# Kernel tuning notes

Measured on AMD Instinct MI355X. Metric: run time of the kernel, lower is better.

## Reference

```python
import jax, jax.numpy as jnp
import numpy as np

V, D, M = 13000, 300, 500   # vocab, embed dim, cell/mem size (hardcoded in source)
B, NW, T = 64, 5, 128       # episodes, ways, seq len
EPS = 1e-8                  # torch cosine_similarity default eps


def setup_inputs():
    key = jax.random.key(0)
    ks = jax.random.split(key, 14)
    s = 0.05  # xavier-ish scale
    return {
        "support_tokens": jax.random.randint(ks[0], (B, NW, T), 0, V, dtype=jnp.int32),
        "target_tokens": jax.random.randint(ks[1], (B, T), 0, V, dtype=jnp.int32),
        "blank_pos_support": jax.random.randint(ks[2], (B, NW), 0, T, dtype=jnp.int32),
        "blank_pos_target": jax.random.randint(ks[3], (B,), 0, T, dtype=jnp.int32),
        "target_y": jax.random.randint(ks[4], (B,), 0, NW, dtype=jnp.int32),
        "emb": jax.random.normal(ks[5], (V, D)) * s,
        "WL": jax.random.normal(ks[6], (3, M, D)) * s,
        "UL": jax.random.normal(ks[7], (3, M, M)) * s,
        "bL": jnp.zeros((3, M)),
        "WR": jax.random.normal(ks[8], (3, M, D)) * s,
        "UR": jax.random.normal(ks[9], (3, M, M)) * s,
        "bR": jnp.zeros((3, M)),
        "Wo": jax.random.normal(ks[10], (D, M)) * s,
        "Uo": jax.random.normal(ks[11], (D, M)) * s,
        "bo": jnp.zeros((D,)),
        "c0L": jnp.zeros((M,)),
        "c0R": jnp.zeros((M,)),
    }


def _cell_scan(x, W, U, b, c0):
    # x: [T, D] -> pre-update cell states (the 'env' the source appends BEFORE updating _c): [T, M]
    gx = jnp.einsum('td,gmd->tgm', x, W) + b  # input projections for all 3 gates, all timesteps
    def step(c, g):
        g = g + jnp.einsum('gmh,h->gm', U, c)
        f = jax.nn.sigmoid(g[0])
        i = jax.nn.sigmoid(g[1])
        cbar = jnp.tanh(g[2])
        return f * c + i * cbar, c
    _, pre = jax.lax.scan(step, c0, gx)
    return pre


def _blank_env(tokens, blank_pos, emb, WL, UL, bL, WR, UR, bR, Wo, Uo, bo, c0L, c0R):
    # tokens: [N, T], blank_pos: [N] -> env vector at blank position: [N, D]
    x = emb[tokens]  # [N, T, D]
    Lenv = jax.vmap(lambda xs: _cell_scan(xs, WL, UL, bL, c0L))(x)          # [N, T, M]
    Renv = jax.vmap(lambda xs: _cell_scan(xs[::-1], WR, UR, bR, c0R))(x)[:, ::-1]
    n = jnp.arange(tokens.shape[0])
    l = Lenv[n, blank_pos]  # [N, M]
    r = Renv[n, blank_pos]  # source pairs Lenv[i] with Renv[T-1-i] of the reversed list == right pre-state at pos i
    return jnp.tanh(l @ Wo.T + r @ Uo.T + bo)  # oNN: unbatched_Linear(lev=0, tanh)


def reference(support_tokens, target_tokens, blank_pos_support, blank_pos_target,
              target_y, emb, WL, UL, bL, WR, UR, bR, Wo, Uo, bo, c0L, c0R):
    b, nw, t = support_tokens.shape
    sup = _blank_env(support_tokens.reshape(b * nw, t), blank_pos_support.reshape(b * nw),
                     emb, WL, UL, bL, WR, UR, bR, Wo, Uo, bo, c0L, c0R).reshape(b, nw, -1)
    tgt = _blank_env(target_tokens, blank_pos_target,
                     emb, WL, UL, bL, WR, UR, bR, Wo, Uo, bo, c0L, c0R)  # [B, D]
    # cosine similarity per way, scaled by 10 (fce LSTM output is discarded in the source, so omitted)
    dot = jnp.einsum('bnd,bd->bn', sup, tgt)
    denom = jnp.maximum(jnp.linalg.norm(sup, axis=-1) * jnp.linalg.norm(tgt, axis=-1)[:, None], EPS)
    z = (dot / denom) * 10.0  # [B, NW]
    probs = jax.nn.softmax(z, axis=1)
    accuracy = jnp.mean((jnp.argmax(probs, axis=1) == target_y).astype(jnp.float32))
    # F.cross_entropy applied to the softmax probs (double softmax), as in the source
    logp = jax.nn.log_softmax(probs, axis=1)
    loss = -jnp.mean(jnp.take_along_axis(logp, target_y[:, None].astype(jnp.int32), axis=1))
    return accuracy, loss
```

## Files before the change

### kernel.cpp

```cpp
#include <hip/hip_runtime.h>
#include <math.h>

#define V 13000
#define D 300
#define M 500
#define B 64
#define NW 5
#define T 128
#define NSUP (B*NW)
#define NSEQ (NSUP + B)
#define CT 32
#define NCT 12
#define MT 16
#define NMT 32
#define KSPL 4
#define CHK 20
#define CKS 10
#define XCH 15
#define NSTEP (T-1)
#define ASZ (KSPL*CHK*MT*4)
#define BSZ (KSPL*CHK*CT)

__device__ __forceinline__ float sigmoidf_(float x){ return 1.0f/(1.0f+expf(-x)); }


__global__ void init_kernel(const float* __restrict__ c0L, const float* __restrict__ c0R,
                            float* __restrict__ actB0, float* __restrict__ c_final)
{
    int idx = blockIdx.x*256 + threadIdx.x;
    if (idx >= 2*M*NSEQ) return;
    int d = idx / (M*NSEQ);
    int rem = idx % (M*NSEQ);
    int m = rem / NSEQ;
    int r = rem % NSEQ;
    float v = d ? c0R[m] : c0L[m];
    actB0[((size_t)d*M + m)*NSEQ + r] = v;
    c_final[((size_t)d*NSEQ + r)*M + m] = v;
}

__global__ void sort_kernel(const int* __restrict__ blank_sup, const int* __restrict__ blank_tgt,
                            int* __restrict__ perm, int* __restrict__ lenR, int* __restrict__ tmax)
{
    __shared__ int L0[NSEQ], L1[NSEQ];
    int tid = threadIdx.x;
    int blank = (tid < NSUP) ? blank_sup[tid] : blank_tgt[tid - NSUP];
    int l0 = blank, l1 = (T-1) - blank;
    L0[tid] = l0; L1[tid] = l1;
    __syncthreads();
    int r0 = 0, r1 = 0;
    for (int j = 0; j < NSEQ; ++j) {
        int c = L0[j]; r0 += (c > l0) || (c == l0 && j < tid);
        int d = L1[j]; r1 += (d > l1) || (d == l1 && j < tid);
    }
    perm[r0] = tid;        lenR[r0] = l0;
    perm[NSEQ + r1] = tid; lenR[NSEQ + r1] = l1;
    __syncthreads();
    if (tid < 2*NCT) {
        int dir = tid / NCT, t = tid % NCT;
        tmax[tid] = lenR[dir*NSEQ + t*CT];
    }
}

__global__ __launch_bounds__(256)
void step_kernel(int s,
                 const float* __restrict__ actB_cur, float* __restrict__ actB_next,
                 float* __restrict__ c_final,
                 const float* __restrict__ WL, const float* __restrict__ UL, const float* __restrict__ bL,
                 const float* __restrict__ WR, const float* __restrict__ UR, const float* __restrict__ bR,
                 const int* __restrict__ perm, const int* __restrict__ lenR, const int* __restrict__ tmax,
                 const int* __restrict__ sup_tok, const int* __restrict__ tgt_tok,
                 const float* __restrict__ emb)
{
    const int bid = blockIdx.x;
    const int ct = bid >> 6;
    const int dm = bid & 63;
    const int d  = dm >> 5;
    const int mt = dm & 31;
    if (s >= tmax[d*NCT + ct]) return;

    __shared__ float smem[ASZ + BSZ];
    __shared__ int tok_s[CT], len_s[CT];

    const int tid  = threadIdx.x;
    const int ks   = tid >> 6;
    const int lane = tid & 63;
    const int ty   = lane >> 3;
    const int tx   = lane & 7;
    const int rank0 = ct*CT;

    if (tid < CT) {
        int rank = rank0 + tid;
        int ch = perm[d*NSEQ + rank];
        len_s[tid] = lenR[d*NSEQ + rank];
        int tpos = d ? (T-1-s) : s;
        tok_s[tid] = (ch < NSUP) ? sup_tok[ch*T + tpos] : tgt_tok[(ch-NSUP)*T + tpos];
    }
    __syncthreads();

    const float* Wd = d ? WR : WL;
    const float* Ud = d ? UR : UL;
    const float* bias = d ? bR : bL;

    float* As = smem;
    float* Bs = smem + ASZ;

    float acc[2][3][4];
    #pragma unroll
    for (int j=0;j<2;++j)
        #pragma unroll
        for (int g=0;g<3;++g)
            #pragma unroll
            for (int c=0;c<4;++c) acc[j][g][c] = 0.f;

    float4 aR[4];
    float4 bR4[3];

    auto loadA = [&](int gc){
        const bool isx = (gc < XCH);
        const int k0 = gc*CHK;
        #pragma unroll
        for (int i=0;i<4;++i){
            int slot = lane + 64*i;
            if (slot < 240){
                int row = slot/5, kq = slot%5;
                int g = row >> 4, ml = row & 15;
                int m = mt*MT + ml;
                float4 v = make_float4(0.f,0.f,0.f,0.f);
                if (m < M){
                    const float* src = isx ? (Wd + (size_t)(g*M + m)*D + k0 + kq*4)
                                           : (Ud + (size_t)(g*M + m)*M + (k0-300) + kq*4);
                    v = *(const float4*)src;
                }
                aR[i] = v;
            }
        }
    };
    auto loadB = [&](int gc){
        const int k0 = gc*CHK;
        if (gc < XCH){
            #pragma unroll
            for (int i=0;i<3;++i){
                int slot = lane + 64*i;
                if (slot < 160){
                    int c = slot/5, kq = slot%5;
                    bR4[i] = *(const float4*)(emb + (size_t)tok_s[c]*D + k0 + kq*4);
                }
            }
        } else {
            #pragma unroll
            for (int i=0;i<3;++i){
                int slot = lane + 64*i;
                if (slot < 160){
                    int kk = slot >> 3, c4 = slot & 7;
                    bR4[i] = *(const float4*)(actB_cur + ((size_t)d*M + (k0-300) + kk)*NSEQ + rank0 + c4*4);
                }
            }
        }
    };
    auto writeAB = [&](int gc){
        #pragma unroll
        for (int i=0;i<4;++i){
            int slot = lane + 64*i;
            if (slot < 240){
                int row = slot/5, kq = slot%5;
                int g = row >> 4, ml = row & 15;
                float4 v = aR[i];
                As[((ks*CHK + kq*4+0)*MT + ml)*4 + g] = v.x;
                As[((ks*CHK + kq*4+1)*MT + ml)*4 + g] = v.y;
                As[((ks*CHK + kq*4+2)*MT + ml)*4 + g] = v.z;
                As[((ks*CHK + kq*4+3)*MT + ml)*4 + g] = v.w;
            }
        }
        if (gc < XCH){
            #pragma unroll
            for (int i=0;i<3;++i){
                int slot = lane + 64*i;
                if (slot < 160){
                    int c = slot/5, kq = slot%5;
                    float4 v = bR4[i];
                    Bs[(ks*CHK + kq*4+0)*CT + c] = v.x;
                    Bs[(ks*CHK + kq*4+1)*CT + c] = v.y;
                    Bs[(ks*CHK + kq*4+2)*CT + c] = v.z;
                    Bs[(ks*CHK + kq*4+3)*CT + c] = v.w;
                }
            }
        } else {
            #pragma unroll
            for (int i=0;i<3;++i){
                int slot = lane + 64*i;
                if (slot < 160){
                    int kk = slot >> 3, c4 = slot & 7;
                    *(float4*)&Bs[(ks*CHK + kk)*CT + c4*4] = bR4[i];
                }
            }
        }
    };

#define FMA4(AC, AV, BV) AC[0] += (AV)*(BV).x; AC[1] += (AV)*(BV).y; AC[2] += (AV)*(BV).z; AC[3] += (AV)*(BV).w;

    loadA(ks*CKS); loadB(ks*CKS);
    for (int ck = 0; ck < CKS; ++ck){
        const int gc = ks*CKS + ck;
        writeAB(gc);
        if (ck + 1 < CKS){ loadA(gc+1); loadB(gc+1); }
        #pragma unroll
        for (int kk = 0; kk < CHK; ++kk){
            float4 a0 = *(const float4*)&As[((ks*CHK + kk)*MT + ty*2    )*4];
            float4 a1 = *(const float4*)&As[((ks*CHK + kk)*MT + ty*2 + 1)*4];
            float4 b  = *(const float4*)&Bs[(ks*CHK + kk)*CT + tx*4];
            FMA4(acc[0][0], a0.x, b);
            FMA4(acc[0][1], a0.y, b);
            FMA4(acc[0][2], a0.z, b);
            FMA4(acc[1][0], a1.x, b);
            FMA4(acc[1][1], a1.y, b);
            FMA4(acc[1][2], a1.z, b);
        }
    }

    __syncthreads();
    float* red = smem;
    #pragma unroll
    for (int j=0;j<2;++j){
        int ml = ty*2 + j;
        #pragma unroll
        for (int g=0;g<3;++g){
            *(float4*)&red[((ks*MT + ml)*3 + g)*CT + tx*4] =
                make_float4(acc[j][g][0], acc[j][g][1], acc[j][g][2], acc[j][g][3]);
        }
    }
    __syncthreads();

    #pragma unroll
    for (int q=0;q<2;++q){
        int cell = tid*2 + q;
        int ml = cell >> 5, c = cell & 31;
        int m = mt*MT + ml;
        if (m < M){
            float g0 = bias[m], g1 = bias[M + m], g2 = bias[2*M + m];
            #pragma unroll
            for (int kq=0;kq<KSPL;++kq){
                g0 += red[((kq*MT + ml)*3 + 0)*CT + c];
                g1 += red[((kq*MT + ml)*3 + 1)*CT + c];
                g2 += red[((kq*MT + ml)*3 + 2)*CT + c];
            }
            int rank = rank0 + c;
            int len  = len_s[c];
            size_t cidx = ((size_t)d*M + m)*NSEQ + rank;
            float cold = actB_cur[cidx];
            float f  = sigmoidf_(g0);
            float i2 = sigmoidf_(g1);
            float cb = tanhf(g2);
            float cn = (s < len) ? (f*cold + i2*cb) : cold;
            actB_next[cidx] = cn;
            if (s == len - 1){
                int ch = perm[d*NSEQ + rank];
                c_final[((size_t)d*NSEQ + ch)*M + m] = cn;
            }
        }
    }
#undef FMA4
}

__global__ void env_kernel(const float* __restrict__ l_states, const float* __restrict__ r_states,
                           const float* __restrict__ Wo, const float* __restrict__ Uo,
                           const float* __restrict__ bo,
                           float* __restrict__ env)
{
    __shared__ __align__(16) float l[M];
    __shared__ __align__(16) float r[M];
    const int i = blockIdx.x;
    const int tid = threadIdx.x;
    for (int m=tid; m<M; m+=blockDim.x){ l[m]=l_states[i*M+m]; r[m]=r_states[i*M+m]; }
    __syncthreads();
    for (int d=tid; d<D; d+=blockDim.x) {
        const float4* wo = reinterpret_cast<const float4*>(Wo + (size_t)d*M);
        const float4* uo = reinterpret_cast<const float4*>(Uo + (size_t)d*M);
        const float4* lv = reinterpret_cast<const float4*>(l);
        const float4* rv = reinterpret_cast<const float4*>(r);
        float acc = bo[d];
        #pragma unroll 5
        for (int q=0; q<M/4; ++q) {
            float4 a=wo[q], bv=lv[q], u=uo[q], rr=rv[q];
            acc += a.x*bv.x + a.y*bv.y + a.z*bv.z + a.w*bv.w;
            acc += u.x*rr.x + u.y*rr.y + u.z*rr.z + u.w*rr.w;
        }
        env[i*D + d] = tanhf(acc);
    }
}

__global__ void episode_kernel(const float* __restrict__ env, const int* __restrict__ target_y,
                               float* __restrict__ flags, float* __restrict__ losses)
{
    const int b = blockIdx.x;
    const int lane = threadIdx.x;
    const float* tgt = env + (size_t)(NSUP + b)*D;

    float tn = 0.f;
    for (int d=lane; d<D; d+=64){ float v=tgt[d]; tn += v*v; }
    for (int off=32; off; off>>=1) tn += __shfl_down(tn, off);
    tn = __shfl(tn, 0);

    float z[NW];
    for (int n=0; n<NW; ++n){
        const float* sup = env + (size_t)(b*NW + n)*D;
        float dot=0.f, sn=0.f;
        for (int d=lane; d<D; d+=64){ float sv=sup[d], tv=tgt[d]; dot+=sv*tv; sn+=sv*sv; }
        for (int off=32; off; off>>=1){ dot += __shfl_down(dot,off); sn += __shfl_down(sn,off); }
        dot = __shfl(dot,0); sn = __shfl(sn,0);
        float denom = fmaxf(sqrtf(sn)*sqrtf(tn), 1e-8f);
        z[n] = dot/denom*10.0f;
    }

    if (lane==0){
        float mx=z[0];
        for(int n=1;n<NW;n++) mx=fmaxf(mx,z[n]);
        float se=0.f; float p[NW];
        for(int n=0;n<NW;n++){ p[n]=expf(z[n]-mx); se+=p[n]; }
        for(int n=0;n<NW;n++) p[n]/=se;
        int am=0; float bv=p[0];
        for(int n=1;n<NW;n++) if(p[n]>bv){bv=p[n];am=n;}
        int y = target_y[b];
        flags[b] = (am==y)?1.0f:0.0f;
        float mx2=p[0]; for(int n=1;n<NW;n++) mx2=fmaxf(mx2,p[n]);
        float se2=0.f; for(int n=0;n<NW;n++) se2+=expf(p[n]-mx2);
        losses[b] = -(p[y]-mx2-logf(se2));
    }
}

__global__ void finalize_kernel(const float* __restrict__ flags, const float* __restrict__ losses,
                                float* __restrict__ out)
{
    const int lane = threadIdx.x;
    float f = flags[lane], l = losses[lane];
    for (int off=32; off; off>>=1){ f += __shfl_down(f,off); l += __shfl_down(l,off); }
    if (lane==0){ out[0] = f/(float)B; out[1] = l/(float)B; }
}

extern "C" void kernel_launch(void* const* d_in, const int* in_sizes, int n_in,
                              void* d_out, int out_size, void* d_ws, size_t ws_size,
                              hipStream_t stream) {
    const int*   sup_tok   = (const int*)d_in[0];
    const int*   tgt_tok   = (const int*)d_in[1];
    const int*   blank_sup = (const int*)d_in[2];
    const int*   blank_tgt = (const int*)d_in[3];
    const int*   target_y  = (const int*)d_in[4];
    const float* emb = (const float*)d_in[5];
    const float* WL  = (const float*)d_in[6];
    const float* UL  = (const float*)d_in[7];
    const float* bL  = (const float*)d_in[8];
    const float* WR  = (const float*)d_in[9];
    const float* UR  = (const float*)d_in[10];
    const float* bR  = (const float*)d_in[11];
    const float* Wo  = (const float*)d_in[12];
    const float* Uo  = (const float*)d_in[13];
    const float* bo  = (const float*)d_in[14];
    const float* c0L = (const float*)d_in[15];
    const float* c0R = (const float*)d_in[16];

    float* ws_f = (float*)d_ws;
    float* actB0   = ws_f;
    float* actB1   = actB0 + 2*M*NSEQ;
    float* c_final = actB1 + 2*M*NSEQ;
    float* env     = c_final + 2*NSEQ*M;
    float* flags   = env + NSEQ*D;
    float* losses  = flags + B;
    int*   perm    = (int*)(losses + B);
    int*   lenR    = perm + 2*NSEQ;
    int*   tmax    = lenR + 2*NSEQ;

    init_kernel<<<(2*M*NSEQ + 255)/256, 256, 0, stream>>>(c0L, c0R, actB0, c_final);
    sort_kernel<<<1, NSEQ, 0, stream>>>(blank_sup, blank_tgt, perm, lenR, tmax);

    for (int s = 0; s < NSTEP; ++s) {
        float* cur  = (s & 1) ? actB1 : actB0;
        float* next = (s & 1) ? actB0 : actB1;
        step_kernel<<<NCT*64, 256, 0, stream>>>(s, cur, next, c_final,
                                                WL, UL, bL, WR, UR, bR,
                                                perm, lenR, tmax, sup_tok, tgt_tok, emb);
    }

    env_kernel<<<NSEQ, 256, 0, stream>>>(c_final, c_final + NSEQ*M, Wo, Uo, bo, env);
    episode_kernel<<<B, 64, 0, stream>>>(env, target_y, flags, losses);
    finalize_kernel<<<1, 64, 0, stream>>>(flags, losses, (float*)d_out);
}
```

Baseline: 5.244 ms.

## Pre-gather next-step embeddings into unified activation buffer and retile GEMM with padded smem

Adds gather blocks to each step launch that copy the next timestep's embedding columns into a combined [x; c] activation buffer (KROW=800 rows), so the compute blocks read the x part and the cell state with the same coalesced, column-major float4 load path instead of token-indexed gathers. Shared memory is reorganized into per-k-split padded strides (ASTR=49, BSTR=36) with precomputed source and destination pointers, and the per-thread tile changes from 2x4 to 4x2 outputs. An extra launch primes the gather for step 0. This adds more blocks per launch and a larger workspace, in exchange for removing the scattered embedding loads and transposed shared-memory writes from the recurrent critical path.

```diff
diff --git a/kernel.cpp b/kernel.cpp
--- a/kernel.cpp
+++ b/kernel.cpp
@@ -12,14 +12,18 @@
 #define CT 32
 #define NCT 12
 #define MT 16
-#define NMT 32
 #define KSPL 4
 #define CHK 20
 #define CKS 10
-#define XCH 15
+#define KROW 800
 #define NSTEP (T-1)
-#define ASZ (KSPL*CHK*MT*4)
-#define BSZ (KSPL*CHK*CT)
+#define ASTR 49
+#define BSTR 36
+#define APW (CHK*ASTR)
+#define BPW (CHK*BSTR)
+#define SMSZ (KSPL*(APW+BPW))
+#define NCOMP 768
+#define NGATH (2*NSEQ)
 
 __device__ __forceinline__ float sigmoidf_(float x){ return 1.0f/(1.0f+expf(-x)); }
 
@@ -34,7 +38,7 @@
     int m = rem / NSEQ;
     int r = rem % NSEQ;
     float v = d ? c0R[m] : c0L[m];
-    actB0[((size_t)d*M + m)*NSEQ + r] = v;
+    actB0[((size_t)d*KROW + 300 + m)*NSEQ + r] = v;
     c_final[((size_t)d*NSEQ + r)*M + m] = v;
 }
 
@@ -72,193 +76,172 @@
                  const float* __restrict__ emb)
 {
     const int bid = blockIdx.x;
+    if (bid >= NCOMP) {
+        const int gb = bid - NCOMP;
+        const int d = gb / NSEQ;
+        const int rank = gb % NSEQ;
+        const int sn = s + 1;
+        if (sn >= NSTEP) return;
+        if (sn >= tmax[d*NCT + (rank >> 5)]) return;
+        const int ch = perm[d*NSEQ + rank];
+        const int tpos = d ? (T-1 - sn) : sn;
+        const int tok = (ch < NSUP) ? sup_tok[ch*T + tpos] : tgt_tok[(ch-NSUP)*T + tpos];
+        const float* src = emb + (size_t)tok*D;
+        float* dst = actB_next + (size_t)d*KROW*NSEQ + rank;
+        for (int k = threadIdx.x; k < D; k += 256) dst[(size_t)k*NSEQ] = src[k];
+        return;
+    }
+    if (s < 0) return;
     const int ct = bid >> 6;
     const int dm = bid & 63;
     const int d  = dm >> 5;
     const int mt = dm & 31;
     if (s >= tmax[d*NCT + ct]) return;
 
-    __shared__ float smem[ASZ + BSZ];
-    __shared__ int tok_s[CT], len_s[CT];
+    __shared__ float smem[SMSZ];
 
     const int tid  = threadIdx.x;
     const int ks   = tid >> 6;
     const int lane = tid & 63;
-    const int ty   = lane >> 3;
-    const int tx   = lane & 7;
+    const int ty   = lane >> 4;
+    const int tx   = lane & 15;
     const int rank0 = ct*CT;
-
-    if (tid < CT) {
-        int rank = rank0 + tid;
-        int ch = perm[d*NSEQ + rank];
-        len_s[tid] = lenR[d*NSEQ + rank];
-        int tpos = d ? (T-1-s) : s;
-        tok_s[tid] = (ch < NSUP) ? sup_tok[ch*T + tpos] : tgt_tok[(ch-NSUP)*T + tpos];
-    }
-    __syncthreads();
 
     const float* Wd = d ? WR : WL;
     const float* Ud = d ? UR : UL;
     const float* bias = d ? bR : bL;
 
-    float* As = smem;
-    float* Bs = smem + ASZ;
-
-    float acc[2][3][4];
-    #pragma unroll
-    for (int j=0;j<2;++j)
-        #pragma unroll
-        for (int g=0;g<3;++g)
-            #pragma unroll
-            for (int c=0;c<4;++c) acc[j][g][c] = 0.f;
-
-    float4 aR[4];
-    float4 bR4[3];
-
+    float* As = smem + ks*APW;
+    float* Bs = smem + KSPL*APW + ks*BPW;
+
+    int aRow[4], aKq[4]; bool aVal[4];
+    const float* aSrcW[4]; const float* aSrcU[4];
+    float* aDst[4];
+    #pragma unroll
+    for (int i = 0; i < 4; ++i) {
+        int slot = lane + 64*i;
+        aVal[i] = (slot < 240);
+        int row = aVal[i] ? slot/5 : 0;
+        int kq  = aVal[i] ? slot%5 : 0;
+        aRow[i] = row; aKq[i] = kq;
+        int g = row >> 4, ml = row & 15;
+        int m = mt*MT + ml; if (m >= M) m = M-1;
+        aSrcW[i] = Wd + (size_t)(g*M + m)*D + kq*4;
+        aSrcU[i] = Ud + (size_t)(g*M + m)*M + kq*4;
+        aDst[i]  = As + kq*4*ASTR + g*16 + ml;
+    }
+    bool bVal[3]; const float* bSrc[3]; float* bDst[3];
+    #pragma unroll
+    for (int i = 0; i < 3; ++i) {
+        int slot = lane + 64*i;
+        bVal[i] = (slot < 160);
+        int kk = (slot < 160 ? slot : 0) >> 3;
+        int c4 = (slot < 160 ? slot : 0) & 7;
+        bSrc[i] = actB_cur + ((size_t)d*KROW + kk)*NSEQ + rank0 + c4*4;
+        bDst[i] = Bs + kk*BSTR + c4*4;
+    }
+
+    float4 aR4[4]; float4 bR4[3];
     auto loadA = [&](int gc){
-        const bool isx = (gc < XCH);
         const int k0 = gc*CHK;
-        #pragma unroll
-        for (int i=0;i<4;++i){
-            int slot = lane + 64*i;
-            if (slot < 240){
-                int row = slot/5, kq = slot%5;
-                int g = row >> 4, ml = row & 15;
-                int m = mt*MT + ml;
-                float4 v = make_float4(0.f,0.f,0.f,0.f);
-                if (m < M){
-                    const float* src = isx ? (Wd + (size_t)(g*M + m)*D + k0 + kq*4)
-                                           : (Ud + (size_t)(g*M + m)*M + (k0-300) + kq*4);
-                    v = *(const float4*)src;
-                }
-                aR[i] = v;
+        const bool isx = (gc < 15);
+        #pragma unroll
+        for (int i = 0; i < 4; ++i)
+            if (aVal[i]) aR4[i] = *(const float4*)(isx ? (aSrcW[i] + k0) : (aSrcU[i] + (k0-300)));
+    };
+    auto loadB = [&](int gc){
+        const size_t ofs = (size_t)(gc*CHK)*NSEQ;
+        #pragma unroll
+        for (int i = 0; i < 3; ++i)
+            if (bVal[i]) bR4[i] = *(const float4*)(bSrc[i] + ofs);
+    };
+    auto writeAB = [&](){
+        #pragma unroll
+        for (int i = 0; i < 4; ++i) {
+            if (aVal[i]) {
+                float* p = aDst[i];
+                p[0*ASTR] = aR4[i].x; p[1*ASTR] = aR4[i].y;
+                p[2*ASTR] = aR4[i].z; p[3*ASTR] = aR4[i].w;
             }
         }
+        #pragma unroll
+        for (int i = 0; i < 3; ++i)
+            if (bVal[i]) *(float4*)bDst[i] = bR4[i];
     };
-    auto loadB = [&](int gc){
-        const int k0 = gc*CHK;
-        if (gc < XCH){
-            #pragma unroll
-            for (int i=0;i<3;++i){
-                int slot = lane + 64*i;
-                if (slot < 160){
-                    int c = slot/5, kq = slot%5;
-                    bR4[i] = *(const float4*)(emb + (size_t)tok_s[c]*D + k0 + kq*4);
-                }
-            }
-        } else {
-            #pragma unroll
-            for (int i=0;i<3;++i){
-                int slot = lane + 64*i;
-                if (slot < 160){
-                    int kk = slot >> 3, c4 = slot & 7;
-                    bR4[i] = *(const float4*)(actB_cur + ((size_t)d*M + (k0-300) + kk)*NSEQ + rank0 + c4*4);
-                }
-            }
+
+    float2 acc[4][3];
+    #pragma unroll
+    for (int j=0;j<4;++j)
+        #pragma unroll
+        for (int g=0;g<3;++g) acc[j][g] = make_float2(0.f,0.f);
+
+    const float* Ard = As + ty*4;
+    const float* Brd = Bs + tx*2;
+
+    loadA(ks*CKS); loadB(ks*CKS);
+    for (int ck = 0; ck < CKS; ++ck) {
+        writeAB();
+        if (ck + 1 < CKS) { loadA(ks*CKS + ck + 1); loadB(ks*CKS + ck + 1); }
+        #pragma unroll
+        for (int kk = 0; kk < CHK; ++kk) {
+            float4 a0 = *(const float4*)(Ard + kk*ASTR);
+            float4 a1 = *(const float4*)(Ard + kk*ASTR + 16);
+            float4 a2 = *(const float4*)(Ard + kk*ASTR + 32);
+            float2 b  = *(const float2*)(Brd + kk*BSTR);
+            acc[0][0].x += a0.x*b.x; acc[0][0].y += a0.x*b.y;
+            acc[1][0].x += a0.y*b.x; acc[1][0].y += a0.y*b.y;
+            acc[2][0].x += a0.z*b.x; acc[2][0].y += a0.z*b.y;
+            acc[3][0].x += a0.w*b.x; acc[3][0].y += a0.w*b.y;
+            acc[0][1].x += a1.x*b.x; acc[0][1].y += a1.x*b.y;
+            acc[1][1].x += a1.y*b.x; acc[1][1].y += a1.y*b.y;
+            acc[2][1].x += a1.z*b.x; acc[2][1].y += a1.z*b.y;
+            acc[3][1].x += a1.w*b.x; acc[3][1].y += a1.w*b.y;
+            acc[0][2].x += a2.x*b.x; acc[0][2].y += a2.x*b.y;
+            acc[1][2].x += a2.y*b.x; acc[1][2].y += a2.y*b.y;
+            acc[2][2].x += a2.z*b.x; acc[2][2].y += a2.z*b.y;
+            acc[3][2].x += a2.w*b.x; acc[3][2].y += a2.w*b.y;
         }
-    };
-    auto writeAB = [&](int gc){
-        #pragma unroll
-        for (int i=0;i<4;++i){
-            int slot = lane + 64*i;
-            if (slot < 240){
-                int row = slot/5, kq = slot%5;
-                int g = row >> 4, ml = row & 15;
-                float4 v = aR[i];
-                As[((ks*CHK + kq*4+0)*MT + ml)*4 + g] = v.x;
-                As[((ks*CHK + kq*4+1)*MT + ml)*4 + g] = v.y;
-                As[((ks*CHK + kq*4+2)*MT + ml)*4 + g] = v.z;
-                As[((ks*CHK + kq*4+3)*MT + ml)*4 + g] = v.w;
-            }
-        }
-        if (gc < XCH){
-            #pragma unroll
-            for (int i=0;i<3;++i){
-                int slot = lane + 64*i;
-                if (slot < 160){
-                    int c = slot/5, kq = slot%5;
-                    float4 v = bR4[i];
-                    Bs[(ks*CHK + kq*4+0)*CT + c] = v.x;
-                    Bs[(ks*CHK + kq*4+1)*CT + c] = v.y;
-                    Bs[(ks*CHK + kq*4+2)*CT + c] = v.z;
-                    Bs[(ks*CHK + kq*4+3)*CT + c] = v.w;
-                }
-            }
-        } else {
-            #pragma unroll
-            for (int i=0;i<3;++i){
-                int slot = lane + 64*i;
-                if (slot < 160){
-                    int kk = slot >> 3, c4 = slot & 7;
-                    *(float4*)&Bs[(ks*CHK + kk)*CT + c4*4] = bR4[i];
-                }
-            }
-        }
-    };
-
-#define FMA4(AC, AV, BV) AC[0] += (AV)*(BV).x; AC[1] += (AV)*(BV).y; AC[2] += (AV)*(BV).z; AC[3] += (AV)*(BV).w;
-
-    loadA(ks*CKS); loadB(ks*CKS);
-    for (int ck = 0; ck < CKS; ++ck){
-        const int gc = ks*CKS + ck;
-        writeAB(gc);
-        if (ck + 1 < CKS){ loadA(gc+1); loadB(gc+1); }
-        #pragma unroll
-        for (int kk = 0; kk < CHK; ++kk){
-            float4 a0 = *(const float4*)&As[((ks*CHK + kk)*MT + ty*2    )*4];
-            float4 a1 = *(const float4*)&As[((ks*CHK + kk)*MT + ty*2 + 1)*4];
-            float4 b  = *(const float4*)&Bs[(ks*CHK + kk)*CT + tx*4];
-            FMA4(acc[0][0], a0.x, b);
-            FMA4(acc[0][1], a0.y, b);
-            FMA4(acc[0][2], a0.z, b);
-            FMA4(acc[1][0], a1.x, b);
-            FMA4(acc[1][1], a1.y, b);
-            FMA4(acc[1][2], a1.z, b);
-        }
     }
 
     __syncthreads();
     float* red = smem;
     #pragma unroll
-    for (int j=0;j<2;++j){
-        int ml = ty*2 + j;
-        #pragma unroll
-        for (int g=0;g<3;++g){
-            *(float4*)&red[((ks*MT + ml)*3 + g)*CT + tx*4] =
-                make_float4(acc[j][g][0], acc[j][g][1], acc[j][g][2], acc[j][g][3]);
-        }
-    }
-    __syncthreads();
-
-    #pragma unroll
-    for (int q=0;q<2;++q){
+    for (int j=0;j<4;++j) {
+        int ml = ty*4 + j;
+        #pragma unroll
+        for (int g=0;g<3;++g)
+            *(float2*)&red[((ks*MT + ml)*3 + g)*CT + tx*2] = acc[j][g];
+    }
+    __syncthreads();
+
+    #pragma unroll
+    for (int q=0;q<2;++q) {
         int cell = tid*2 + q;
         int ml = cell >> 5, c = cell & 31;
         int m = mt*MT + ml;
-        if (m < M){
+        if (m < M) {
             float g0 = bias[m], g1 = bias[M + m], g2 = bias[2*M + m];
             #pragma unroll
-            for (int kq=0;kq<KSPL;++kq){
+            for (int kq=0;kq<KSPL;++kq) {
                 g0 += red[((kq*MT + ml)*3 + 0)*CT + c];
                 g1 += red[((kq*MT + ml)*3 + 1)*CT + c];
                 g2 += red[((kq*MT + ml)*3 + 2)*CT + c];
             }
             int rank = rank0 + c;
-            int len  = len_s[c];
-            size_t cidx = ((size_t)d*M + m)*NSEQ + rank;
+            int len  = lenR[d*NSEQ + rank];
+            size_t cidx = ((size_t)d*KROW + 300 + m)*NSEQ + rank;
             float cold = actB_cur[cidx];
             float f  = sigmoidf_(g0);
             float i2 = sigmoidf_(g1);
             float cb = tanhf(g2);
             float cn = (s < len) ? (f*cold + i2*cb) : cold;
             actB_next[cidx] = cn;
-            if (s == len - 1){
+            if (s == len - 1) {
                 int ch = perm[d*NSEQ + rank];
                 c_final[((size_t)d*NSEQ + ch)*M + m] = cn;
             }
         }
     }
-#undef FMA4
 }
 
 __global__ void env_kernel(const float* __restrict__ l_states, const float* __restrict__ r_states,
@@ -357,10 +340,11 @@
     const float* c0L = (const float*)d_in[15];
     const float* c0R = (const float*)d_in[16];
 
+    const size_t ACTSZ = (size_t)2*KROW*NSEQ;
     float* ws_f = (float*)d_ws;
     float* actB0   = ws_f;
-    float* actB1   = actB0 + 2*M*NSEQ;
-    float* c_final = actB1 + 2*M*NSEQ;
+    float* actB1   = actB0 + ACTSZ;
+    float* c_final = actB1 + ACTSZ;
     float* env     = c_final + 2*NSEQ*M;
     float* flags   = env + NSEQ*D;
     float* losses  = flags + B;
@@ -371,12 +355,15 @@
     init_kernel<<<(2*M*NSEQ + 255)/256, 256, 0, stream>>>(c0L, c0R, actB0, c_final);
     sort_kernel<<<1, NSEQ, 0, stream>>>(blank_sup, blank_tgt, perm, lenR, tmax);
 
+    step_kernel<<<NCOMP + NGATH, 256, 0, stream>>>(-1, actB1, actB0, c_final,
+                                                   WL, UL, bL, WR, UR, bR,
+                                                   perm, lenR, tmax, sup_tok, tgt_tok, emb);
     for (int s = 0; s < NSTEP; ++s) {
         float* cur  = (s & 1) ? actB1 : actB0;
         float* next = (s & 1) ? actB0 : actB1;
-        step_kernel<<<NCT*64, 256, 0, stream>>>(s, cur, next, c_final,
-                                                WL, UL, bL, WR, UR, bR,
-                                                perm, lenR, tmax, sup_tok, tgt_tok, emb);
+        step_kernel<<<NCOMP + NGATH, 256, 0, stream>>>(s, cur, next, c_final,
+                                                       WL, UL, bL, WR, UR, bR,
+                                                       perm, lenR, tmax, sup_tok, tgt_tok, emb);
     }
 
     env_kernel<<<NSEQ, 256, 0, stream>>>(c_final, c_final + NSEQ*M, Wo, Uo, bo, env);
```

New measurement: 14.96 ms. 2.85x slower.
